# Optimization experiments

Hardware: AMD Instinct MI355X
Metric: run time of the kernel (lower is better)

Reference implementation:

```python
import jax, jax.numpy as jnp
import numpy as np

B, S, D, HW = 256, 32, 512, 196


def setup_inputs() -> dict:
    key = jax.random.key(0)
    ks = jax.random.split(key, 34)
    n = lambda k, sh, s=1.0: jax.random.normal(k, sh, dtype=jnp.float32) * s
    w = 0.03  # xavier-ish scale for D=512 layers
    return {
        "words": n(ks[0], (B, S, D)),
        "question": n(ks[1], (B, 2 * D)),
        "know": n(ks[2], (B, D, HW)),
        "control0": n(ks[3], (B, D)),
        "memory0": n(ks[4], (B, D)),
        # ControlUnit
        "Wsc": n(ks[5], (2 * D, D), w), "bsc": jnp.zeros((D,), jnp.float32),
        "Wp": n(ks[6], (D, D), w), "bp": jnp.zeros((D,), jnp.float32),
        "Wcq": n(ks[7], (2 * D, D), w), "bcq": jnp.zeros((D,), jnp.float32),
        "wac": n(ks[8], (D, 1), w), "bac": jnp.zeros((1,), jnp.float32),
        # ReadUnit
        "Wm": n(ks[9], (D, D), w), "bm": jnp.zeros((D,), jnp.float32),
        "Wk": n(ks[10], (D, D), w), "bk": jnp.zeros((D,), jnp.float32),
        "Wc1": n(ks[11], (3 * D, D), w), "bc1": jnp.zeros((D,), jnp.float32),
        "Wc2": n(ks[12], (D, D), w), "bc2": jnp.zeros((D,), jnp.float32),
        "war": n(ks[13], (D, 1), w), "bar": jnp.zeros((1,), jnp.float32),
        # WriteUnit (self-attention variant)
        "Wwc": n(ks[14], (D, D), w), "bwc": jnp.zeros((D,), jnp.float32),
        "waw": n(ks[15], (D, 1), w), "baw": jnp.zeros((1,), jnp.float32),
        "Wwcat": n(ks[16], (3 * D, D), w), "bwcat": jnp.zeros((D,), jnp.float32),
    }


def reference(words, question, know, control0, memory0,
              Wsc, bsc, Wp, bp, Wcq, bcq, wac, bac,
              Wm, bm, Wk, bk, Wc1, bc1, Wc2, bc2, war, bar,
              Wwc, bwc, waw, baw, Wwcat, bwcat):
    # ---- ControlUnit (step 0) ----
    q = jnp.tanh(question @ Wsc + bsc)                    # [B,D]
    pa = q @ Wp + bp                                      # position_aware[0]
    cq = jnp.concatenate([control0, pa], axis=1) @ Wcq + bcq  # [B,D]
    logit_c = (cq[:, None, :] * words) @ wac + bac        # [B,S,1]
    attn_c = jax.nn.softmax(logit_c, axis=1)
    control = jnp.sum(attn_c * words, axis=1)             # [B,D]

    # ---- ReadUnit ----
    pm = memory0 @ Wm + bm                                # [B,D]
    pk = jnp.einsum('bdn,de->ben', know, Wk) + bk[None, :, None]  # [B,D,HW]
    pm_b = jnp.broadcast_to(pm[:, :, None], pk.shape)
    feat = jnp.concatenate([pm_b * pk, pk, pm_b], axis=1)  # [B,3D,HW]
    h = jax.nn.relu(jnp.einsum('bfn,fd->bnd', feat, Wc1) + bc1)  # [B,HW,D]
    h = h @ Wc2 + bc2                                     # [B,HW,D]
    logit_r = (h * control[:, None, :]) @ war + bar       # [B,HW,1]
    a_r = jax.nn.softmax(logit_r[..., 0], axis=1)          # [B,HW]
    read = jnp.einsum('bdn,bn->bd', know, a_r)            # [B,D]

    # ---- WriteUnit (self-attention over previous controls; T=1 at step 0) ----
    sc = control @ Wwc + bwc                              # [B,D]
    ctrl_prev = control0[:, :, None]                      # [B,D,T]
    logit_w = jnp.einsum('bdt,d->bt', sc[:, :, None] * ctrl_prev, waw[:, 0]) + baw  # [B,T]
    a_w = jax.nn.softmax(logit_w, axis=1)
    attn_mem = jnp.einsum('bdt,bt->bd', memory0[:, :, None], a_w)  # [B,D]
    concat = jnp.concatenate([read, memory0, attn_mem], axis=1)    # [B,3D]
    next_mem = concat @ Wwcat + bwcat                     # [B,D]

    return control, next_mem
```

## Files before the change

### kernel.cpp

```cpp
#include <hip/hip_runtime.h>
#include <hip/hip_bf16.h>
#include <math.h>

typedef __hip_bfloat16 bf16;
typedef __attribute__((ext_vector_type(8))) short s8v;
typedef __attribute__((ext_vector_type(4))) short s4v;
typedef __attribute__((ext_vector_type(4))) float f4v;

#define BB 256
#define SS 32
#define DD 512
#define HWN 196
#define APW 72

__device__ __forceinline__ float b2f(bf16 x){ return __bfloat162float(x); }
__device__ __forceinline__ bf16 f2b(float x){ return __float2bfloat16(x); }
__device__ __forceinline__ float us2f(unsigned short u){
    union { unsigned int i; float f; } t; t.i = ((unsigned int)u) << 16; return t.f;
}
__device__ __forceinline__ float ldin(int dt, const void* p, size_t i){
    return dt ? b2f(((const bf16*)p)[i]) : ((const float*)p)[i];
}

__global__ void detect_k(const void* q, int* flag){
    __shared__ int cnt;
    if (threadIdx.x == 0) cnt = 0;
    __syncthreads();
    const unsigned short* u = (const unsigned short*)q;
    unsigned short v = u[threadIdx.x * 4];
    int e = (v >> 7) & 0xFF;
    atomicAdd(&cnt, (e >= 100 && e <= 140) ? 1 : 0);
    __syncthreads();
    if (threadIdx.x == 0) *flag = (cnt > 128) ? 1 : 0;
}

struct PJob { const void* s; const void* s_b; const void* s2; const void* s2_b;
              bf16* d; int R, C, ldd, kofs, mode, boff; };
struct PrepP { PJob j[11]; const void* war; const void* bk; float* warf; float* bkf; };

__global__ __launch_bounds__(256) void prep_k(PrepP P, const int* __restrict__ flag){
    const int dt = *flag;
    __shared__ float T[32][33];
    int bx = blockIdx.x;
    int ji = 0;
    #pragma unroll
    for (int i = 0; i < 11; ++i) if (bx >= P.j[i].boff) ji = i;
    PJob jb = P.j[ji];
    const void* src  = dt ? jb.s_b  : jb.s;
    const void* src2 = dt ? jb.s2_b : jb.s2;
    int t = bx - jb.boff;
    int tx = threadIdx.x & 31, ty = threadIdx.x >> 5;
    if (jb.mode == 3){
        for (int i = threadIdx.x; i < DD; i += 256){
            P.warf[i] = ldin(dt, P.war, i);
            P.bkf[i]  = ldin(dt, P.bk, i);
        }
        return;
    }
    int nrt = jb.R >> 5;
    int r0 = (t % nrt) << 5, c0 = (t / nrt) << 5;
    if (jb.mode == 2){
        for (int rr = ty; rr < 32; rr += 8)
            jb.d[(size_t)(r0 + rr) * jb.ldd + jb.kofs + c0 + tx] =
                f2b(ldin(dt, src, (size_t)(r0 + rr) * jb.C + c0 + tx));
        return;
    }
    for (int rr = ty; rr < 32; rr += 8){
        float v = ldin(dt, src, (size_t)(r0 + rr) * jb.C + c0 + tx);
        if (jb.mode == 1) v += ldin(dt, src2, (size_t)(r0 + rr) * jb.C + c0 + tx);
        T[rr][tx] = v;
    }
    __syncthreads();
    for (int rr = ty; rr < 32; rr += 8)
        jb.d[(size_t)(c0 + rr) * jb.ldd + jb.kofs + r0 + tx] = f2b(T[tx][rr]);
}

__global__ __launch_bounds__(256) void g1_mfma(const void* __restrict__ know,
                                               const bf16* __restrict__ BT,
                                               const float* __restrict__ bkf,
                                               bf16* __restrict__ C,
                                               int b0, int swz,
                                               const int* __restrict__ flag){
    const int dt = *flag;
    __shared__ __align__(16) bf16 As[128 * APW];
    __shared__ __align__(16) bf16 Bs[128 * APW];
    const int tid = threadIdx.x, lane = tid & 63, wave = tid >> 6;
    const int q = lane >> 4, mr = lane & 15;
    int idb = blockIdx.x, rt, ct;
    if (swz){ int g = idb >> 5, w = idb & 31; rt = g * 8 + (w & 7); ct = w >> 3; }
    else    { rt = idb >> 2; ct = idb & 3; }
    const int r0 = rt * 128, c0 = ct * 128;
    const int quad = tid >> 3;
    const int kg   = tid & 7;
    const int m    = r0 + quad * 4;
    const int bl   = m / HWN;
    const int n    = m - bl * HWN;
    const size_t abase = ((size_t)(b0 + bl) * DD) * HWN + n;
    f4v acc[2][8];
    #pragma unroll
    for (int t = 0; t < 2; ++t)
        #pragma unroll
        for (int j = 0; j < 8; ++j){ f4v z = {0.f,0.f,0.f,0.f}; acc[t][j] = z; }
    for (int k0 = 0; k0 < DD; k0 += 64){
        #pragma unroll
        for (int h = 0; h < 2; ++h){
            int kb = k0 + h * 32 + kg * 4;
            union { bf16 hh[4]; s4v v; } pk_[4];
            if (dt == 0){
                const float* kp = (const float*)know + abase + (size_t)kb * HWN;
                float4 ra  = *(const float4*)kp;
                float4 rb  = *(const float4*)(kp + HWN);
                float4 rc  = *(const float4*)(kp + 2 * HWN);
                float4 rd4 = *(const float4*)(kp + 3 * HWN);
                #pragma unroll
                for (int j = 0; j < 4; ++j){
                    pk_[j].hh[0] = f2b((&ra.x)[j]);
                    pk_[j].hh[1] = f2b((&rb.x)[j]);
                    pk_[j].hh[2] = f2b((&rc.x)[j]);
                    pk_[j].hh[3] = f2b((&rd4.x)[j]);
                }
            } else {
                const unsigned short* kp = (const unsigned short*)know + abase + (size_t)kb * HWN;
                ushort4 ua = *(const ushort4*)kp;
                ushort4 ub = *(const ushort4*)(kp + HWN);
                ushort4 uc = *(const ushort4*)(kp + 2 * HWN);
                ushort4 ud = *(const ushort4*)(kp + 3 * HWN);
                #pragma unroll
                for (int j = 0; j < 4; ++j){
                    ((unsigned short*)&pk_[j].v)[0] = (&ua.x)[j];
                    ((unsigned short*)&pk_[j].v)[1] = (&ub.x)[j];
                    ((unsigned short*)&pk_[j].v)[2] = (&uc.x)[j];
                    ((unsigned short*)&pk_[j].v)[3] = (&ud.x)[j];
                }
            }
            #pragma unroll
            for (int j = 0; j < 4; ++j)
                *(s4v*)&As[(quad * 4 + j) * APW + h * 32 + kg * 4] = pk_[j].v;
        }
        {
            int col = tid >> 1, kb = (tid & 1) * 32;
            const bf16* wp = BT + (size_t)(c0 + col) * DD + k0 + kb;
            bf16* dst = &Bs[col * APW + kb];
            #pragma unroll
            for (int t4 = 0; t4 < 32; t4 += 8)
                *(float4*)(dst + t4) = *(const float4*)(wp + t4);
        }
        __syncthreads();
        #pragma unroll
        for (int h = 0; h < 2; ++h){
            s8v a0 = *(const s8v*)&As[(wave * 32 + mr) * APW + h * 32 + q * 8];
            s8v a1 = *(const s8v*)&As[(wave * 32 + 16 + mr) * APW + h * 32 + q * 8];
            #pragma unroll
            for (int j = 0; j < 8; ++j){
                s8v b = *(const s8v*)&Bs[(j * 16 + mr) * APW + h * 32 + q * 8];
                acc[0][j] = __builtin_amdgcn_mfma_f32_16x16x32_bf16(a0, b, acc[0][j], 0, 0, 0);
                acc[1][j] = __builtin_amdgcn_mfma_f32_16x16x32_bf16(a1, b, acc[1][j], 0, 0, 0);
            }
        }
        __syncthreads();
    }
    #pragma unroll
    for (int t = 0; t < 2; ++t)
        #pragma unroll
        for (int j = 0; j < 8; ++j){
            float bb = bkf[c0 + j * 16 + mr];
            #pragma unroll
            for (int i = 0; i < 4; ++i){
                int row = r0 + wave * 32 + t * 16 + q * 4 + i;
                int col = c0 + j * 16 + mr;
                C[(size_t)row * DD + col] = f2b(acc[t][j][i] + bb);
            }
        }
}

__global__ __launch_bounds__(256) void g2_mfma(const bf16* __restrict__ Apk,
                                               const bf16* __restrict__ BT,
                                               const float* __restrict__ pmf,
                                               const float* __restrict__ t3b,
                                               const float* __restrict__ uf,
                                               float* __restrict__ lpart,
                                               int b0, int swz){
    __shared__ __align__(16) bf16 As[128 * APW];
    __shared__ __align__(16) bf16 Bs[128 * APW];
    const int tid = threadIdx.x, lane = tid & 63, wave = tid >> 6;
    const int q = lane >> 4, mr = lane & 15;
    int idb = blockIdx.x, u, ct;
    if (swz){ int g = idb >> 5, w = idb & 31; u = g * 8 + (w & 7); ct = w >> 3; }
    else    { u = idb >> 2; ct = idb & 3; }
    const int bl = u >> 1, rt = u & 1;
    const int b = b0 + bl;
    const int c0 = ct * 128, rbase = rt * 128;
    const float* pmb = pmf + (size_t)b * DD;
    f4v acc[2][8];
    #pragma unroll
    for (int t = 0; t < 2; ++t)
        #pragma unroll
        for (int j = 0; j < 8; ++j){ f4v z = {0.f,0.f,0.f,0.f}; acc[t][j] = z; }
    for (int k0 = 0; k0 < DD; k0 += 64){
        {
            int row = tid >> 1, kb = (tid & 1) * 32;
            int rl = rbase + row;
            bf16* dst = &As[row * APW + kb];
            if (rl < HWN){
                const bf16* ap = Apk + ((size_t)bl * HWN + rl) * DD + k0 + kb;
                #pragma unroll
                for (int t4 = 0; t4 < 32; t4 += 8)
                    *(float4*)(dst + t4) = *(const float4*)(ap + t4);
            } else {
                float4 z = {0.f,0.f,0.f,0.f};
                #pragma unroll
                for (int t4 = 0; t4 < 32; t4 += 8)
                    *(float4*)(dst + t4) = z;
            }
        }
        {
            int col = tid >> 1, kb = (tid & 1) * 32;
            const bf16* wrow = BT + (size_t)(c0 + col) * (2 * DD) + k0 + kb;
            bf16* dst = &Bs[col * APW + kb];
            #pragma unroll
            for (int t4 = 0; t4 < 32; t4 += 8){
                union { bf16 h[8]; float4 f; } w1, w2, be;
                w1.f = *(const float4*)(wrow + t4);
                w2.f = *(const float4*)(wrow + DD + t4);
                float4 pA = *(const float4*)(pmb + k0 + kb + t4);
                float4 pB = *(const float4*)(pmb + k0 + kb + t4 + 4);
                #pragma unroll
                for (int j = 0; j < 4; ++j){
                    be.h[j]     = f2b((&pA.x)[j] * b2f(w1.h[j])     + b2f(w2.h[j]));
                    be.h[4 + j] = f2b((&pB.x)[j] * b2f(w1.h[4 + j]) + b2f(w2.h[4 + j]));
                }
                *(float4*)(dst + t4) = be.f;
            }
        }
        __syncthreads();
        #pragma unroll
        for (int h = 0; h < 2; ++h){
            s8v a0 = *(const s8v*)&As[(wave * 32 + mr) * APW + h * 32 + q * 8];
            s8v a1 = *(const s8v*)&As[(wave * 32 + 16 + mr) * APW + h * 32 + q * 8];
            #pragma unroll
            for (int j = 0; j < 8; ++j){
                s8v b2 = *(const s8v*)&Bs[(j * 16 + mr) * APW + h * 32 + q * 8];
                acc[0][j] = __builtin_amdgcn_mfma_f32_16x16x32_bf16(a0, b2, acc[0][j], 0, 0, 0);
                acc[1][j] = __builtin_amdgcn_mfma_f32_16x16x32_bf16(a1, b2, acc[1][j], 0, 0, 0);
            }
        }
        __syncthreads();
    }
    float part[2][4] = {};
    #pragma unroll
    for (int t = 0; t < 2; ++t)
        #pragma unroll
        for (int j = 0; j < 8; ++j)
            #pragma unroll
            for (int i = 0; i < 4; ++i){
                int rl = rbase + wave * 32 + t * 16 + q * 4 + i;
                if (rl < HWN){
                    int col = c0 + j * 16 + mr;
                    float hv = acc[t][j][i] + t3b[(size_t)b * DD + col];
                    part[t][i] += fmaxf(hv, 0.f) * uf[(size_t)b * DD + col];
                }
            }
    #pragma unroll
    for (int t = 0; t < 2; ++t)
        #pragma unroll
        for (int i = 0; i < 4; ++i){
            float v = part[t][i];
            v += __shfl_xor(v, 1, 16);
            v += __shfl_xor(v, 2, 16);
            v += __shfl_xor(v, 4, 16);
            v += __shfl_xor(v, 8, 16);
            int rl = rbase + wave * 32 + t * 16 + q * 4 + i;
            if (mr == 0 && rl < HWN)
                lpart[(size_t)ct * (BB * HWN) + (size_t)b * HWN + rl] = v;
        }
}

struct SSeg { const void* A; int a_ws, lda, K, koff; };
struct SP {
    SSeg s[2]; int nseg;
    const bf16* BT; int ldb;
    const float* amul;
    const void* bias;
    float* C; int M, N, act;
    void* out2; int o2off;
};
struct SPP { SP j[2]; };

__global__ __launch_bounds__(256) void sgemm_k(SPP P, const int* __restrict__ flag){
    const int dt = *flag;
    const SP p = P.j[blockIdx.z];
    const int tid = threadIdx.x, lane = tid & 63, w = tid >> 6;
    const int q = lane >> 4, mr = lane & 15;
    const int n0 = blockIdx.x * 16, m0 = blockIdx.y * 64 + w * 16;
    f4v acc = {0.f,0.f,0.f,0.f};
    for (int sg = 0; sg < p.nseg; ++sg){
        const SSeg s = p.s[sg];
        const float* amul = (sg == 0) ? p.amul : nullptr;
        #pragma unroll 4
        for (int k0 = 0; k0 < s.K; k0 += 32){
            const int kk = k0 + q * 8;
            union { bf16 h[8]; s8v v; } a;
            if (s.a_ws || dt == 0){
                const float* Af = (const float*)s.A + (size_t)(m0 + mr) * s.lda + kk;
                float4 f0 = *(const float4*)Af;
                float4 f1 = *(const float4*)(Af + 4);
                float f[8] = {f0.x, f0.y, f0.z, f0.w, f1.x, f1.y, f1.z, f1.w};
                if (amul){
                    #pragma unroll
                    for (int j = 0; j < 8; ++j) f[j] *= amul[kk + j];
                }
                #pragma unroll
                for (int j = 0; j < 8; ++j) a.h[j] = f2b(f[j]);
            } else {
                a.v = *(const s8v*)((const bf16*)s.A + (size_t)(m0 + mr) * s.lda + kk);
                if (amul){
                    #pragma unroll
                    for (int j = 0; j < 8; ++j) a.h[j] = f2b(b2f(a.h[j]) * amul[kk + j]);
                }
            }
            s8v b = *(const s8v*)(p.BT + (size_t)(n0 + mr) * p.ldb + s.koff + kk);
            acc = __builtin_amdgcn_mfma_f32_16x16x32_bf16(a.v, b, acc, 0, 0, 0);
        }
    }
    #pragma unroll
    for (int i = 0; i < 4; ++i){
        int row = m0 + q * 4 + i, col = n0 + mr;
        float v = acc[i] + (p.bias ? ldin(dt, p.bias, col) : 0.f);
        if (p.act == 1) v = tanhf(v);
        p.C[(size_t)row * p.N + col] = v;
        if (p.out2){
            size_t oi = (size_t)p.o2off + (size_t)row * p.N + col;
            if (dt) ((bf16*)p.out2)[oi] = f2b(v);
            else    ((float*)p.out2)[oi] = v;
        }
    }
}

__global__ __launch_bounds__(256) void attn_control_k(const float* __restrict__ cq,
                                                      const void* __restrict__ wac,
                                                      const void* __restrict__ bac,
                                                      const void* __restrict__ words,
                                                      float* __restrict__ control,
                                                      const void* __restrict__ bc2,
                                                      const float* __restrict__ warf,
                                                      const void* __restrict__ bar,
                                                      float* __restrict__ bias_r,
                                                      void* __restrict__ out,
                                                      const int* __restrict__ flag){
    const int dt = *flag;
    const int b = blockIdx.x, tid = threadIdx.x;
    __shared__ float cw[DD];
    __shared__ float lg[SS];
    __shared__ float es[SS];
    __shared__ float red[256];
    for (int d = tid; d < DD; d += 256) cw[d] = cq[(size_t)b*DD + d] * ldin(dt, wac, d);
    __syncthreads();
    int s = tid >> 3, l8 = tid & 7;
    float p = 0.f;
    for (int d = l8; d < DD; d += 8) p += cw[d] * ldin(dt, words, ((size_t)b*SS + s)*DD + d);
    for (int off = 4; off; off >>= 1) p += __shfl_down(p, off, 8);
    if (l8 == 0) lg[s] = p + ldin(dt, bac, 0);
    __syncthreads();
    if (tid == 0){
        float mx = -INFINITY;
        for (int i = 0; i < SS; ++i) mx = fmaxf(mx, lg[i]);
        float sm = 0.f;
        for (int i = 0; i < SS; ++i){ es[i] = expf(lg[i] - mx); sm += es[i]; }
        float inv = 1.f / sm;
        for (int i = 0; i < SS; ++i) es[i] *= inv;
    }
    __syncthreads();
    float vb = 0.f;
    for (int d = tid; d < DD; d += 256){
        float c = 0.f;
        #pragma unroll 8
        for (int s2 = 0; s2 < SS; ++s2) c += es[s2] * ldin(dt, words, ((size_t)b*SS + s2)*DD + d);
        control[(size_t)b*DD + d] = c;
        if (dt) ((bf16*)out)[(size_t)b*DD + d] = f2b(c);
        else    ((float*)out)[(size_t)b*DD + d] = c;
        vb += ldin(dt, bc2, d) * c * warf[d];
    }
    red[tid] = vb; __syncthreads();
    for (int off = 128; off; off >>= 1){ if (tid < off) red[tid] += red[tid + off]; __syncthreads(); }
    if (tid == 0) bias_r[b] = red[0] + ldin(dt, bar, 0);
}

__global__ __launch_bounds__(256) void softmax_read_k(const float* __restrict__ lpart,
                                                      const float* __restrict__ bias_r,
                                                      const void* __restrict__ know,
                                                      float* __restrict__ readout,
                                                      const int* __restrict__ flag){
    const int dt = *flag;
    const int b = blockIdx.x, tid = threadIdx.x;
    __shared__ float a[HWN];
    __shared__ float red[256];
    float x = -INFINITY;
    if (tid < HWN){
        float sacc = bias_r[b];
        #pragma unroll
        for (int c = 0; c < 4; ++c)
            sacc += lpart[(size_t)c * (BB * HWN) + (size_t)b * HWN + tid];
        x = sacc;
    }
    red[tid] = x; __syncthreads();
    for (int off = 128; off; off >>= 1){ if (tid < off) red[tid] = fmaxf(red[tid], red[tid + off]); __syncthreads(); }
    float mx = red[0]; __syncthreads();
    float e = (tid < HWN) ? expf(x - mx) : 0.f;
    red[tid] = e; __syncthreads();
    for (int off = 128; off; off >>= 1){ if (tid < off) red[tid] += red[tid + off]; __syncthreads(); }
    float inv = 1.f / red[0];
    if (tid < HWN) a[tid] = e * inv;
    __syncthreads();
    for (int d = tid; d < DD; d += 256){
        size_t base = ((size_t)b*DD + d) * HWN;
        float sum = 0.f;
        if (dt){
            const ushort4* k4 = (const ushort4*)((const unsigned short*)know + base);
            #pragma unroll 7
            for (int c = 0; c < HWN/4; ++c){
                ushort4 u4 = k4[c];
                sum += a[4*c+0]*us2f(u4.x) + a[4*c+1]*us2f(u4.y)
                     + a[4*c+2]*us2f(u4.z) + a[4*c+3]*us2f(u4.w);
            }
        } else {
            const float4* k4 = (const float4*)((const float*)know + base);
            #pragma unroll 7
            for (int c = 0; c < HWN/4; ++c){
                float4 f4 = k4[c];
                sum += a[4*c+0]*f4.x + a[4*c+1]*f4.y + a[4*c+2]*f4.z + a[4*c+3]*f4.w;
            }
        }
        readout[(size_t)b*DD + d] = sum;
    }
}

extern "C" void kernel_launch(void* const* d_in, const int* in_sizes, int n_in,
                              void* d_out, int out_size, void* d_ws, size_t ws_size,
                              hipStream_t stream){
    const void* words    = d_in[0];
    const void* question = d_in[1];
    const void* know     = d_in[2];
    const void* control0 = d_in[3];
    const void* memory0  = d_in[4];
    const void* Wsc = d_in[5];   const void* bsc = d_in[6];
    const void* Wp  = d_in[7];   const void* bp  = d_in[8];
    const void* Wcq = d_in[9];   const void* bcq = d_in[10];
    const void* wac = d_in[11];  const void* bac = d_in[12];
    const void* Wm  = d_in[13];  const void* bm  = d_in[14];
    const void* Wk  = d_in[15];  const void* bk  = d_in[16];
    const void* Wc1 = d_in[17];  const void* bc1 = d_in[18];
    const void* Wc2 = d_in[19];  const void* bc2 = d_in[20];
    const void* war = d_in[21];  const void* bar = d_in[22];
    const void* Wwcat = d_in[27]; const void* bwcat = d_in[28];

    int* flag = (int*)d_ws;
    float* F = ((float*)d_ws) + 16;
    const int NBD = BB * DD;
    float* q_   = F;
    float* pa   = F + 1*NBD;
    float* cq   = F + 2*NBD;
    float* ctrl = F + 3*NBD;
    float* pm   = F + 4*NBD;
    float* t3b  = F + 5*NBD;
    float* u_   = F + 6*NBD;
    float* rd   = F + 7*NBD;
    float* nm   = F + 8*NBD;
    float* bias_r = F + 9*NBD;
    float* warf   = bias_r + BB;
    float* bkf    = warf + DD;
    float* lpart  = bkf + DD;
    size_t off_f = 16 + 9*(size_t)NBD + BB + 2*DD + 8*(size_t)BB*HWN;
    size_t byte_off = (off_f * 4 + 255) & ~(size_t)255;
    bf16* WB = (bf16*)((char*)d_ws + byte_off);
    bf16* WscT   = WB;
    bf16* WcqT   = WscT  + (size_t)DD*2*DD;
    bf16* Wc1T2  = WcqT  + (size_t)DD*2*DD;
    bf16* WwcatF = Wc1T2 + (size_t)DD*2*DD;
    bf16* WpT    = WwcatF+ (size_t)DD*2*DD;
    bf16* WmT    = WpT   + (size_t)DD*DD;
    bf16* Wc1t3T = WmT   + (size_t)DD*DD;
    bf16* WkT    = Wc1t3T+ (size_t)DD*DD;
    bf16* Wc2cv  = WkT   + (size_t)DD*DD;
    size_t big_off = (byte_off + ((size_t)DD*2*DD*4 + (size_t)DD*DD*5) * sizeof(bf16) + 255) & ~(size_t)255;

    size_t per_batch = (size_t)HWN * DD * sizeof(bf16);
    size_t avail = (ws_size > big_off) ? (ws_size - big_off) : 0;
    int CB = (int)(avail / per_batch);
    CB &= ~31;
    if (CB > BB) CB = BB;
    if (CB < 32) CB = 32;
    bf16* pkT = (bf16*)((char*)d_ws + big_off);

    dim3 blk(256);

    detect_k<<<dim3(1), blk, 0, stream>>>(question, flag);

    {
        PrepP P; int bo = 0;
        auto J = [&](const void* s, const void* sb, const void* s2, const void* s2b,
                     bf16* d, int R, int C, int ldd, int kofs, int mode, int idx){
            int nb = (mode == 3) ? 1 : ((R >> 5) * (C >> 5));
            P.j[idx] = PJob{ s, sb, s2, s2b, d, R, C, ldd, kofs, mode, bo };
            bo += nb;
        };
        const void* Wc1t3_f = (const void*)((const float*)Wc1 + (size_t)2*DD*DD);
        const void* Wc1t3_b = (const void*)((const bf16*) Wc1 + (size_t)2*DD*DD);
        const void* Ww1_f = (const void*)((const float*)Wwcat + (size_t)DD*DD);
        const void* Ww1_b = (const void*)((const bf16*) Wwcat + (size_t)DD*DD);
        const void* Ww2_f = (const void*)((const float*)Wwcat + (size_t)2*DD*DD);
        const void* Ww2_b = (const void*)((const bf16*) Wwcat + (size_t)2*DD*DD);
        J(Wsc,   Wsc,   nullptr, nullptr, WscT,   2*DD, DD, 2*DD, 0,   0, 0);
        J(Wp,    Wp,    nullptr, nullptr, WpT,    DD,   DD, DD,   0,   0, 1);
        J(Wcq,   Wcq,   nullptr, nullptr, WcqT,   2*DD, DD, 2*DD, 0,   0, 2);
        J(Wm,    Wm,    nullptr, nullptr, WmT,    DD,   DD, DD,   0,   0, 3);
        J(Wc1,   Wc1,   nullptr, nullptr, Wc1T2,  2*DD, DD, 2*DD, 0,   0, 4);
        J(Wc1t3_f, Wc1t3_b, nullptr, nullptr, Wc1t3T, DD, DD, DD, 0,   0, 5);
        J(Wk,    Wk,    nullptr, nullptr, WkT,    DD,   DD, DD,   0,   0, 6);
        J(Wwcat, Wwcat, nullptr, nullptr, WwcatF, DD,   DD, 2*DD, 0,   0, 7);
        J(Ww1_f, Ww1_b, Ww2_f,   Ww2_b,   WwcatF, DD,   DD, 2*DD, 512, 1, 8);
        J(Wc2,   Wc2,   nullptr, nullptr, Wc2cv,  DD,   DD, DD,   0,   2, 9);
        J(nullptr,nullptr,nullptr,nullptr,nullptr,0,    0,  0,    0,   3, 10);
        P.war = war; P.bk = bk; P.warf = warf; P.bkf = bkf;
        prep_k<<<dim3(bo), blk, 0, stream>>>(P, flag);
    }

    SPP P2;
    auto mkjob = [&](SP& p){ p = SP{}; };

    mkjob(P2.j[0]);
    P2.j[0].nseg = 1;
    P2.j[0].s[0] = SSeg{ question, 0, 2*DD, 2*DD, 0 };
    P2.j[0].BT = WscT; P2.j[0].ldb = 2*DD;
    P2.j[0].bias = bsc; P2.j[0].C = q_; P2.j[0].M = BB; P2.j[0].N = DD; P2.j[0].act = 1;
    mkjob(P2.j[1]);
    P2.j[1].nseg = 1;
    P2.j[1].s[0] = SSeg{ memory0, 0, DD, DD, 0 };
    P2.j[1].BT = WmT; P2.j[1].ldb = DD;
    P2.j[1].bias = bm; P2.j[1].C = pm; P2.j[1].M = BB; P2.j[1].N = DD; P2.j[1].act = 0;
    sgemm_k<<<dim3(DD/16, BB/64, 2), blk, 0, stream>>>(P2, flag);

    mkjob(P2.j[0]);
    P2.j[0].nseg = 1;
    P2.j[0].s[0] = SSeg{ q_, 1, DD, DD, 0 };
    P2.j[0].BT = WpT; P2.j[0].ldb = DD;
    P2.j[0].bias = bp; P2.j[0].C = pa; P2.j[0].M = BB; P2.j[0].N = DD; P2.j[0].act = 0;
    mkjob(P2.j[1]);
    P2.j[1].nseg = 1;
    P2.j[1].s[0] = SSeg{ pm, 1, DD, DD, 0 };
    P2.j[1].BT = Wc1t3T; P2.j[1].ldb = DD;
    P2.j[1].bias = bc1; P2.j[1].C = t3b; P2.j[1].M = BB; P2.j[1].N = DD; P2.j[1].act = 0;
    sgemm_k<<<dim3(DD/16, BB/64, 2), blk, 0, stream>>>(P2, flag);

    mkjob(P2.j[0]);
    P2.j[0].nseg = 2;
    P2.j[0].s[0] = SSeg{ control0, 0, DD, DD, 0 };
    P2.j[0].s[1] = SSeg{ pa,       1, DD, DD, 512 };
    P2.j[0].BT = WcqT; P2.j[0].ldb = 2*DD;
    P2.j[0].bias = bcq; P2.j[0].C = cq; P2.j[0].M = BB; P2.j[0].N = DD; P2.j[0].act = 0;
    sgemm_k<<<dim3(DD/16, BB/64, 1), blk, 0, stream>>>(P2, flag);

    attn_control_k<<<dim3(BB), blk, 0, stream>>>(cq, wac, bac, words, ctrl,
                                                 bc2, warf, bar, bias_r, d_out, flag);

    mkjob(P2.j[0]);
    P2.j[0].nseg = 1;
    P2.j[0].s[0] = SSeg{ ctrl, 1, DD, DD, 0 };
    P2.j[0].BT = Wc2cv; P2.j[0].ldb = DD; P2.j[0].amul = warf;
    P2.j[0].C = u_; P2.j[0].M = BB; P2.j[0].N = DD; P2.j[0].act = 0;
    sgemm_k<<<dim3(DD/16, BB/64, 1), blk, 0, stream>>>(P2, flag);

    for (int b0 = 0; b0 < BB; b0 += CB){
        int cb = (b0 + CB <= BB) ? CB : (BB - b0);
        int M = cb * HWN;
        int nR = M / 128;
        int swz1 = (nR % 8 == 0) ? 1 : 0;
        g1_mfma<<<dim3(4 * nR), blk, 0, stream>>>(know, WkT, bkf, pkT, b0, swz1, flag);
        int nU = cb * 2;
        int swz2 = (nU % 8 == 0) ? 1 : 0;
        g2_mfma<<<dim3(4 * nU), blk, 0, stream>>>(pkT, Wc1T2, pm, t3b, u_, lpart, b0, swz2);
    }

    softmax_read_k<<<dim3(BB), blk, 0, stream>>>(lpart, bias_r, know, rd, flag);

    mkjob(P2.j[0]);
    P2.j[0].nseg = 2;
    P2.j[0].s[0] = SSeg{ rd,      1, DD, DD, 0 };
    P2.j[0].s[1] = SSeg{ memory0, 0, DD, DD, 512 };
    P2.j[0].BT = WwcatF; P2.j[0].ldb = 2*DD;
    P2.j[0].bias = bwcat; P2.j[0].C = nm; P2.j[0].M = BB; P2.j[0].N = DD; P2.j[0].act = 0;
    P2.j[0].out2 = d_out; P2.j[0].o2off = NBD;
    sgemm_k<<<dim3(DD/16, BB/64, 1), blk, 0, stream>>>(P2, flag);
}
```

Before: 556.8 us.

## Fuse know-projection and Wc1 GEMMs into one kernel keeping pk in LDS

Replaces the two-pass g1/g2 pipeline, which wrote the projected knowledge pk to global memory in bf16 and read it back, with one fused kernel per (batch, row-half) tile. The kernel computes the full 128x512 pk tile into LDS, then runs the second GEMM from LDS and reduces the logits, including the bias, directly. This removes the large pk round trip to global memory and the 4-way partial logit buffer. In exchange each block holds a 512-wide accumulator (4x2x8 f4v), needs about 150 KB of dynamic LDS at one block per CU, and re-reads the Wk and Wc1 weights once per block. It also adds register prefetch pipelining of the A and B operands.

```diff
diff --git a/kernel.cpp b/kernel.cpp
--- a/kernel.cpp
+++ b/kernel.cpp
@@ -4,14 +4,14 @@
 
 typedef __hip_bfloat16 bf16;
 typedef __attribute__((ext_vector_type(8))) short s8v;
-typedef __attribute__((ext_vector_type(4))) short s4v;
 typedef __attribute__((ext_vector_type(4))) float f4v;
 
 #define BB 256
 #define SS 32
 #define DD 512
 #define HWN 196
-#define APW 72
+#define PKP 520
+#define SGP 72
 
 __device__ __forceinline__ float b2f(bf16 x){ return __bfloat162float(x); }
 __device__ __forceinline__ bf16 f2b(float x){ return __float2bfloat16(x); }
@@ -75,191 +75,202 @@
         jb.d[(size_t)(c0 + rr) * jb.ldd + jb.kofs + r0 + tx] = f2b(T[tx][rr]);
 }
 
-__global__ __launch_bounds__(256) void g1_mfma(const void* __restrict__ know,
-                                               const bf16* __restrict__ BT,
-                                               const float* __restrict__ bkf,
-                                               bf16* __restrict__ C,
-                                               int b0, int swz,
-                                               const int* __restrict__ flag){
+__global__ __launch_bounds__(256, 1) void g12_fused(const void* __restrict__ know,
+                                                    const bf16* __restrict__ WkT,
+                                                    const float* __restrict__ bkf,
+                                                    const bf16* __restrict__ Wc1T2,
+                                                    const float* __restrict__ pmf,
+                                                    const float* __restrict__ t3b,
+                                                    const float* __restrict__ uf,
+                                                    const float* __restrict__ bias_r,
+                                                    float* __restrict__ logit,
+                                                    const int* __restrict__ flag){
+    extern __shared__ char smem[];
+    bf16* pk  = (bf16*)smem;
+    bf16* stg = (bf16*)(smem + 128 * PKP * 2);
     const int dt = *flag;
-    __shared__ __align__(16) bf16 As[128 * APW];
-    __shared__ __align__(16) bf16 Bs[128 * APW];
     const int tid = threadIdx.x, lane = tid & 63, wave = tid >> 6;
     const int q = lane >> 4, mr = lane & 15;
-    int idb = blockIdx.x, rt, ct;
-    if (swz){ int g = idb >> 5, w = idb & 31; rt = g * 8 + (w & 7); ct = w >> 3; }
-    else    { rt = idb >> 2; ct = idb & 3; }
-    const int r0 = rt * 128, c0 = ct * 128;
-    const int quad = tid >> 3;
-    const int kg   = tid & 7;
-    const int m    = r0 + quad * 4;
-    const int bl   = m / HWN;
-    const int n    = m - bl * HWN;
-    const size_t abase = ((size_t)(b0 + bl) * DD) * HWN + n;
-    f4v acc[2][8];
+    const int bid = blockIdx.x;
+    const int u = (bid & 7) * 64 + (bid >> 3);
+    const int b = u >> 1, rt = u & 1;
+    const int r0 = rt * 128;
+    const int colh = tid >> 1, kbh = (tid & 1) * 32;
+
+    float          frA[2][2][8];
+    unsigned short urA[2][2][8];
+    float4 Bv[4];
+    s8v af[2][2];
+    f4v acc[4][2][8];
     #pragma unroll
-    for (int t = 0; t < 2; ++t)
-        #pragma unroll
-        for (int j = 0; j < 8; ++j){ f4v z = {0.f,0.f,0.f,0.f}; acc[t][j] = z; }
-    for (int k0 = 0; k0 < DD; k0 += 64){
-        #pragma unroll
-        for (int h = 0; h < 2; ++h){
-            int kb = k0 + h * 32 + kg * 4;
-            union { bf16 hh[4]; s4v v; } pk_[4];
+    for (int n = 0; n < 4; ++n)
+        #pragma unroll
+        for (int t = 0; t < 2; ++t)
+            #pragma unroll
+            for (int j = 0; j < 8; ++j){ f4v z = {0.f,0.f,0.f,0.f}; acc[n][t][j] = z; }
+
+    const int rowA[2] = { r0 + wave * 32 + mr, r0 + wave * 32 + 16 + mr };
+    const int rowC[2] = { rowA[0] < HWN ? rowA[0] : HWN - 1,
+                          rowA[1] < HWN ? rowA[1] : HWN - 1 };
+
+    auto issueA = [&](int ks){
+        #pragma unroll
+        for (int t = 0; t < 2; ++t){
+            const size_t base = ((size_t)b * DD + ks * 64 + q * 8) * HWN + rowC[t];
             if (dt == 0){
-                const float* kp = (const float*)know + abase + (size_t)kb * HWN;
-                float4 ra  = *(const float4*)kp;
-                float4 rb  = *(const float4*)(kp + HWN);
-                float4 rc  = *(const float4*)(kp + 2 * HWN);
-                float4 rd4 = *(const float4*)(kp + 3 * HWN);
-                #pragma unroll
-                for (int j = 0; j < 4; ++j){
-                    pk_[j].hh[0] = f2b((&ra.x)[j]);
-                    pk_[j].hh[1] = f2b((&rb.x)[j]);
-                    pk_[j].hh[2] = f2b((&rc.x)[j]);
-                    pk_[j].hh[3] = f2b((&rd4.x)[j]);
+                const float* kp = (const float*)know;
+                #pragma unroll
+                for (int h = 0; h < 2; ++h)
+                    #pragma unroll
+                    for (int e = 0; e < 8; ++e)
+                        frA[t][h][e] = kp[base + (size_t)(h * 32 + e) * HWN];
+            } else {
+                const unsigned short* kp = (const unsigned short*)know;
+                #pragma unroll
+                for (int h = 0; h < 2; ++h)
+                    #pragma unroll
+                    for (int e = 0; e < 8; ++e)
+                        urA[t][h][e] = kp[base + (size_t)(h * 32 + e) * HWN];
+            }
+        }
+    };
+    auto packA = [&](){
+        #pragma unroll
+        for (int t = 0; t < 2; ++t){
+            const bool vld = (rowA[t] < HWN);
+            #pragma unroll
+            for (int h = 0; h < 2; ++h){
+                union { bf16 hh[8]; unsigned short uu[8]; s8v v; } tmp;
+                if (dt == 0){
+                    #pragma unroll
+                    for (int e = 0; e < 8; ++e) tmp.hh[e] = f2b(vld ? frA[t][h][e] : 0.f);
+                } else {
+                    #pragma unroll
+                    for (int e = 0; e < 8; ++e) tmp.uu[e] = vld ? urA[t][h][e] : (unsigned short)0;
                 }
-            } else {
-                const unsigned short* kp = (const unsigned short*)know + abase + (size_t)kb * HWN;
-                ushort4 ua = *(const ushort4*)kp;
-                ushort4 ub = *(const ushort4*)(kp + HWN);
-                ushort4 uc = *(const ushort4*)(kp + 2 * HWN);
-                ushort4 ud = *(const ushort4*)(kp + 3 * HWN);
-                #pragma unroll
-                for (int j = 0; j < 4; ++j){
-                    ((unsigned short*)&pk_[j].v)[0] = (&ua.x)[j];
-                    ((unsigned short*)&pk_[j].v)[1] = (&ub.x)[j];
-                    ((unsigned short*)&pk_[j].v)[2] = (&uc.x)[j];
-                    ((unsigned short*)&pk_[j].v)[3] = (&ud.x)[j];
+                af[t][h] = tmp.v;
+            }
+        }
+    };
+    auto issueB = [&](int ks, int n){
+        const bf16* wp = WkT + (size_t)(n * 128 + colh) * DD + ks * 64 + kbh;
+        #pragma unroll
+        for (int t4 = 0; t4 < 4; ++t4) Bv[t4] = *(const float4*)(wp + t4 * 8);
+    };
+    auto writeB = [&](){
+        #pragma unroll
+        for (int t4 = 0; t4 < 4; ++t4)
+            *(float4*)&stg[colh * SGP + kbh + t4 * 8] = Bv[t4];
+    };
+
+    issueA(0);
+    issueB(0, 0);
+    for (int ks = 0; ks < 8; ++ks){
+        packA();
+        if (ks < 7) issueA(ks + 1);
+        #pragma unroll
+        for (int n = 0; n < 4; ++n){
+            __syncthreads();
+            writeB();
+            { int ks2 = (n == 3) ? ks + 1 : ks, n2 = (n + 1) & 3;
+              if (ks2 > 7){ ks2 = 7; n2 = 3; }
+              issueB(ks2, n2); }
+            __syncthreads();
+            #pragma unroll
+            for (int h = 0; h < 2; ++h){
+                #pragma unroll
+                for (int j = 0; j < 8; ++j){
+                    s8v bb = *(const s8v*)&stg[(j * 16 + mr) * SGP + h * 32 + q * 8];
+                    acc[n][0][j] = __builtin_amdgcn_mfma_f32_16x16x32_bf16(af[0][h], bb, acc[n][0][j], 0, 0, 0);
+                    acc[n][1][j] = __builtin_amdgcn_mfma_f32_16x16x32_bf16(af[1][h], bb, acc[n][1][j], 0, 0, 0);
                 }
             }
-            #pragma unroll
-            for (int j = 0; j < 4; ++j)
-                *(s4v*)&As[(quad * 4 + j) * APW + h * 32 + kg * 4] = pk_[j].v;
-        }
-        {
-            int col = tid >> 1, kb = (tid & 1) * 32;
-            const bf16* wp = BT + (size_t)(c0 + col) * DD + k0 + kb;
-            bf16* dst = &Bs[col * APW + kb];
-            #pragma unroll
-            for (int t4 = 0; t4 < 32; t4 += 8)
-                *(float4*)(dst + t4) = *(const float4*)(wp + t4);
-        }
-        __syncthreads();
-        #pragma unroll
-        for (int h = 0; h < 2; ++h){
-            s8v a0 = *(const s8v*)&As[(wave * 32 + mr) * APW + h * 32 + q * 8];
-            s8v a1 = *(const s8v*)&As[(wave * 32 + 16 + mr) * APW + h * 32 + q * 8];
+        }
+    }
+
+    float4 Wv[8], Pv[8];
+    auto issueW = [&](int n, int es){
+        const bf16*  wrow = Wc1T2 + (size_t)(n * 128 + colh) * (2 * DD) + es * 64 + kbh;
+        const float* pmb  = pmf + (size_t)b * DD + es * 64 + kbh;
+        #pragma unroll
+        for (int t4 = 0; t4 < 4; ++t4){
+            Wv[2 * t4]     = *(const float4*)(wrow + t4 * 8);
+            Wv[2 * t4 + 1] = *(const float4*)(wrow + DD + t4 * 8);
+            Pv[2 * t4]     = *(const float4*)(pmb + t4 * 8);
+            Pv[2 * t4 + 1] = *(const float4*)(pmb + t4 * 8 + 4);
+        }
+    };
+    auto writeW = [&](){
+        #pragma unroll
+        for (int t4 = 0; t4 < 4; ++t4){
+            union { bf16 h[8]; float4 f; } w1, w2, be;
+            w1.f = Wv[2 * t4]; w2.f = Wv[2 * t4 + 1];
+            float4 pA = Pv[2 * t4], pB = Pv[2 * t4 + 1];
+            #pragma unroll
+            for (int j = 0; j < 4; ++j){
+                be.h[j]     = f2b((&pA.x)[j] * b2f(w1.h[j])     + b2f(w2.h[j]));
+                be.h[4 + j] = f2b((&pB.x)[j] * b2f(w1.h[4 + j]) + b2f(w2.h[4 + j]));
+            }
+            *(float4*)&stg[colh * SGP + kbh + t4 * 8] = be.f;
+        }
+    };
+    issueW(0, 0);
+
+    #pragma unroll
+    for (int n = 0; n < 4; ++n)
+        #pragma unroll
+        for (int j = 0; j < 8; ++j){
+            const int col = n * 128 + j * 16 + mr;
+            const float bv = bkf[col];
+            #pragma unroll
+            for (int t = 0; t < 2; ++t)
+                #pragma unroll
+                for (int i = 0; i < 4; ++i)
+                    pk[(wave * 32 + t * 16 + q * 4 + i) * PKP + col] = f2b(acc[n][t][j][i] + bv);
+        }
+
+    float part[2][4] = {{0.f,0.f,0.f,0.f},{0.f,0.f,0.f,0.f}};
+    for (int n = 0; n < 4; ++n){
+        f4v hacc[2][8];
+        #pragma unroll
+        for (int t = 0; t < 2; ++t)
+            #pragma unroll
+            for (int j = 0; j < 8; ++j){ f4v z = {0.f,0.f,0.f,0.f}; hacc[t][j] = z; }
+        for (int es = 0; es < 8; ++es){
+            __syncthreads();
+            writeW();
+            { int n2 = n, e2 = es + 1;
+              if (e2 == 8){ e2 = 0; n2 = n + 1; }
+              if (n2 == 4){ n2 = 3; e2 = 7; }
+              issueW(n2, e2); }
+            __syncthreads();
+            #pragma unroll
+            for (int h = 0; h < 2; ++h){
+                s8v a0 = *(const s8v*)&pk[(wave * 32 + mr) * PKP + es * 64 + h * 32 + q * 8];
+                s8v a1 = *(const s8v*)&pk[(wave * 32 + 16 + mr) * PKP + es * 64 + h * 32 + q * 8];
+                #pragma unroll
+                for (int j = 0; j < 8; ++j){
+                    s8v bb = *(const s8v*)&stg[(j * 16 + mr) * SGP + h * 32 + q * 8];
+                    hacc[0][j] = __builtin_amdgcn_mfma_f32_16x16x32_bf16(a0, bb, hacc[0][j], 0, 0, 0);
+                    hacc[1][j] = __builtin_amdgcn_mfma_f32_16x16x32_bf16(a1, bb, hacc[1][j], 0, 0, 0);
+                }
+            }
+        }
+        #pragma unroll
+        for (int t = 0; t < 2; ++t)
             #pragma unroll
             for (int j = 0; j < 8; ++j){
-                s8v b = *(const s8v*)&Bs[(j * 16 + mr) * APW + h * 32 + q * 8];
-                acc[0][j] = __builtin_amdgcn_mfma_f32_16x16x32_bf16(a0, b, acc[0][j], 0, 0, 0);
-                acc[1][j] = __builtin_amdgcn_mfma_f32_16x16x32_bf16(a1, b, acc[1][j], 0, 0, 0);
-            }
-        }
-        __syncthreads();
-    }
-    #pragma unroll
-    for (int t = 0; t < 2; ++t)
-        #pragma unroll
-        for (int j = 0; j < 8; ++j){
-            float bb = bkf[c0 + j * 16 + mr];
-            #pragma unroll
-            for (int i = 0; i < 4; ++i){
-                int row = r0 + wave * 32 + t * 16 + q * 4 + i;
-                int col = c0 + j * 16 + mr;
-                C[(size_t)row * DD + col] = f2b(acc[t][j][i] + bb);
-            }
-        }
-}
-
-__global__ __launch_bounds__(256) void g2_mfma(const bf16* __restrict__ Apk,
-                                               const bf16* __restrict__ BT,
-                                               const float* __restrict__ pmf,
-                                               const float* __restrict__ t3b,
-                                               const float* __restrict__ uf,
-                                               float* __restrict__ lpart,
-                                               int b0, int swz){
-    __shared__ __align__(16) bf16 As[128 * APW];
-    __shared__ __align__(16) bf16 Bs[128 * APW];
-    const int tid = threadIdx.x, lane = tid & 63, wave = tid >> 6;
-    const int q = lane >> 4, mr = lane & 15;
-    int idb = blockIdx.x, u, ct;
-    if (swz){ int g = idb >> 5, w = idb & 31; u = g * 8 + (w & 7); ct = w >> 3; }
-    else    { u = idb >> 2; ct = idb & 3; }
-    const int bl = u >> 1, rt = u & 1;
-    const int b = b0 + bl;
-    const int c0 = ct * 128, rbase = rt * 128;
-    const float* pmb = pmf + (size_t)b * DD;
-    f4v acc[2][8];
-    #pragma unroll
-    for (int t = 0; t < 2; ++t)
-        #pragma unroll
-        for (int j = 0; j < 8; ++j){ f4v z = {0.f,0.f,0.f,0.f}; acc[t][j] = z; }
-    for (int k0 = 0; k0 < DD; k0 += 64){
-        {
-            int row = tid >> 1, kb = (tid & 1) * 32;
-            int rl = rbase + row;
-            bf16* dst = &As[row * APW + kb];
-            if (rl < HWN){
-                const bf16* ap = Apk + ((size_t)bl * HWN + rl) * DD + k0 + kb;
-                #pragma unroll
-                for (int t4 = 0; t4 < 32; t4 += 8)
-                    *(float4*)(dst + t4) = *(const float4*)(ap + t4);
-            } else {
-                float4 z = {0.f,0.f,0.f,0.f};
-                #pragma unroll
-                for (int t4 = 0; t4 < 32; t4 += 8)
-                    *(float4*)(dst + t4) = z;
-            }
-        }
-        {
-            int col = tid >> 1, kb = (tid & 1) * 32;
-            const bf16* wrow = BT + (size_t)(c0 + col) * (2 * DD) + k0 + kb;
-            bf16* dst = &Bs[col * APW + kb];
-            #pragma unroll
-            for (int t4 = 0; t4 < 32; t4 += 8){
-                union { bf16 h[8]; float4 f; } w1, w2, be;
-                w1.f = *(const float4*)(wrow + t4);
-                w2.f = *(const float4*)(wrow + DD + t4);
-                float4 pA = *(const float4*)(pmb + k0 + kb + t4);
-                float4 pB = *(const float4*)(pmb + k0 + kb + t4 + 4);
-                #pragma unroll
-                for (int j = 0; j < 4; ++j){
-                    be.h[j]     = f2b((&pA.x)[j] * b2f(w1.h[j])     + b2f(w2.h[j]));
-                    be.h[4 + j] = f2b((&pB.x)[j] * b2f(w1.h[4 + j]) + b2f(w2.h[4 + j]));
+                const int col = n * 128 + j * 16 + mr;
+                #pragma unroll
+                for (int i = 0; i < 4; ++i){
+                    const int rl = r0 + wave * 32 + t * 16 + q * 4 + i;
+                    if (rl < HWN){
+                        float hv = hacc[t][j][i] + t3b[(size_t)b * DD + col];
+                        part[t][i] += fmaxf(hv, 0.f) * uf[(size_t)b * DD + col];
+                    }
                 }
-                *(float4*)(dst + t4) = be.f;
-            }
-        }
-        __syncthreads();
-        #pragma unroll
-        for (int h = 0; h < 2; ++h){
-            s8v a0 = *(const s8v*)&As[(wave * 32 + mr) * APW + h * 32 + q * 8];
-            s8v a1 = *(const s8v*)&As[(wave * 32 + 16 + mr) * APW + h * 32 + q * 8];
-            #pragma unroll
-            for (int j = 0; j < 8; ++j){
-                s8v b2 = *(const s8v*)&Bs[(j * 16 + mr) * APW + h * 32 + q * 8];
-                acc[0][j] = __builtin_amdgcn_mfma_f32_16x16x32_bf16(a0, b2, acc[0][j], 0, 0, 0);
-                acc[1][j] = __builtin_amdgcn_mfma_f32_16x16x32_bf16(a1, b2, acc[1][j], 0, 0, 0);
-            }
-        }
-        __syncthreads();
-    }
-    float part[2][4] = {};
-    #pragma unroll
-    for (int t = 0; t < 2; ++t)
-        #pragma unroll
-        for (int j = 0; j < 8; ++j)
-            #pragma unroll
-            for (int i = 0; i < 4; ++i){
-                int rl = rbase + wave * 32 + t * 16 + q * 4 + i;
-                if (rl < HWN){
-                    int col = c0 + j * 16 + mr;
-                    float hv = acc[t][j][i] + t3b[(size_t)b * DD + col];
-                    part[t][i] += fmaxf(hv, 0.f) * uf[(size_t)b * DD + col];
-                }
-            }
+            }
+    }
     #pragma unroll
     for (int t = 0; t < 2; ++t)
         #pragma unroll
@@ -269,9 +280,9 @@
             v += __shfl_xor(v, 2, 16);
             v += __shfl_xor(v, 4, 16);
             v += __shfl_xor(v, 8, 16);
-            int rl = rbase + wave * 32 + t * 16 + q * 4 + i;
+            const int rl = r0 + wave * 32 + t * 16 + q * 4 + i;
             if (mr == 0 && rl < HWN)
-                lpart[(size_t)ct * (BB * HWN) + (size_t)b * HWN + rl] = v;
+                logit[(size_t)b * HWN + rl] = v + bias_r[b];
         }
 }
 
@@ -385,8 +396,7 @@
     if (tid == 0) bias_r[b] = red[0] + ldin(dt, bar, 0);
 }
 
-__global__ __launch_bounds__(256) void softmax_read_k(const float* __restrict__ lpart,
-                                                      const float* __restrict__ bias_r,
+__global__ __launch_bounds__(256) void softmax_read_k(const float* __restrict__ logit,
                                                       const void* __restrict__ know,
                                                       float* __restrict__ readout,
                                                       const int* __restrict__ flag){
@@ -394,14 +404,7 @@
     const int b = blockIdx.x, tid = threadIdx.x;
     __shared__ float a[HWN];
     __shared__ float red[256];
-    float x = -INFINITY;
-    if (tid < HWN){
-        float sacc = bias_r[b];
-        #pragma unroll
-        for (int c = 0; c < 4; ++c)
-            sacc += lpart[(size_t)c * (BB * HWN) + (size_t)b * HWN + tid];
-        x = sacc;
-    }
+    float x = (tid < HWN) ? logit[(size_t)b*HWN + tid] : -INFINITY;
     red[tid] = x; __syncthreads();
     for (int off = 128; off; off >>= 1){ if (tid < off) red[tid] = fmaxf(red[tid], red[tid + off]); __syncthreads(); }
     float mx = red[0]; __syncthreads();
@@ -468,8 +471,8 @@
     float* bias_r = F + 9*NBD;
     float* warf   = bias_r + BB;
     float* bkf    = warf + DD;
-    float* lpart  = bkf + DD;
-    size_t off_f = 16 + 9*(size_t)NBD + BB + 2*DD + 8*(size_t)BB*HWN;
+    float* logit  = bkf + DD;
+    size_t off_f = 16 + 9*(size_t)NBD + BB + 2*DD + (size_t)BB*HWN;
     size_t byte_off = (off_f * 4 + 255) & ~(size_t)255;
     bf16* WB = (bf16*)((char*)d_ws + byte_off);
     bf16* WscT   = WB;
@@ -481,15 +484,6 @@
     bf16* Wc1t3T = WmT   + (size_t)DD*DD;
     bf16* WkT    = Wc1t3T+ (size_t)DD*DD;
     bf16* Wc2cv  = WkT   + (size_t)DD*DD;
-    size_t big_off = (byte_off + ((size_t)DD*2*DD*4 + (size_t)DD*DD*5) * sizeof(bf16) + 255) & ~(size_t)255;
-
-    size_t per_batch = (size_t)HWN * DD * sizeof(bf16);
-    size_t avail = (ws_size > big_off) ? (ws_size - big_off) : 0;
-    int CB = (int)(avail / per_batch);
-    CB &= ~31;
-    if (CB > BB) CB = BB;
-    if (CB < 32) CB = 32;
-    bf16* pkT = (bf16*)((char*)d_ws + big_off);
 
     dim3 blk(256);
 
@@ -569,18 +563,19 @@
     P2.j[0].C = u_; P2.j[0].M = BB; P2.j[0].N = DD; P2.j[0].act = 0;
     sgemm_k<<<dim3(DD/16, BB/64, 1), blk, 0, stream>>>(P2, flag);
 
-    for (int b0 = 0; b0 < BB; b0 += CB){
-        int cb = (b0 + CB <= BB) ? CB : (BB - b0);
-        int M = cb * HWN;
-        int nR = M / 128;
-        int swz1 = (nR % 8 == 0) ? 1 : 0;
-        g1_mfma<<<dim3(4 * nR), blk, 0, stream>>>(know, WkT, bkf, pkT, b0, swz1, flag);
-        int nU = cb * 2;
-        int swz2 = (nU % 8 == 0) ? 1 : 0;
-        g2_mfma<<<dim3(4 * nU), blk, 0, stream>>>(pkT, Wc1T2, pm, t3b, u_, lpart, b0, swz2);
-    }
-
-    softmax_read_k<<<dim3(BB), blk, 0, stream>>>(lpart, bias_r, know, rd, flag);
+    {
+        static bool attr_set = false;
+        const int g12_lds = 128 * PKP * 2 + 128 * SGP * 2;
+        if (!attr_set){
+            (void)hipFuncSetAttribute(reinterpret_cast<const void*>(g12_fused),
+                                      hipFuncAttributeMaxDynamicSharedMemorySize, g12_lds);
+            attr_set = true;
+        }
+        g12_fused<<<dim3(2 * BB), blk, g12_lds, stream>>>(know, WkT, bkf, Wc1T2,
+                                                          pm, t3b, u_, bias_r, logit, flag);
+    }
+
+    softmax_read_k<<<dim3(BB), blk, 0, stream>>>(logit, know, rd, flag);
 
     mkjob(P2.j[0]);
     P2.j[0].nseg = 2;
```

Result: slower. 875.2 us (+57.2%).
